# Kernel tuning notes

Hardware: AMD Instinct MI355X
Metric: run time of the kernel (lower is better)

Reference implementation:

```python
import jax, jax.numpy as jnp
import numpy as np


def _hippo_scale_params(N, L):
    """Replicates HiPPOScale.__init__ for discretization='bilinear' (pure numpy)."""
    q = np.arange(N, dtype=np.float64)
    col, row = np.meshgrid(q, q)
    r = 2 * q + 1
    M = -(np.where(row >= col, r, 0) - np.diag(q))
    T = np.sqrt(np.diag(2 * q + 1))
    A = T @ M @ np.linalg.inv(T)          # (N, N)
    B = np.diag(T)                         # (N,)
    ts = np.arange(1, L + 1, dtype=np.float64)[:, None, None]  # (L,1,1)
    At = A[None] / ts                      # A / t, batched over t
    I = np.eye(N, dtype=np.float64)
    Mm = I[None] - 0.5 * At
    Nn = I[None] + 0.5 * At
    A_stacked = np.linalg.solve(Mm, Nn)                      # (L, N, N)
    Bt = B[None, :] / ts[:, 0, :]                             # (L, N)
    B_stacked = np.linalg.solve(Mm, Bt[..., None])[..., 0]    # (L, N)
    return A_stacked.astype(np.float32), B_stacked.astype(np.float32)


def setup_inputs() -> dict:
    N, L, Bsz = 64, 4096, 64
    key = jax.random.key(0)
    A_st, B_st = _hippo_scale_params(N, L)
    inputs = jax.random.normal(key, (L, Bsz), dtype=jnp.float32)
    return {
        "inputs": inputs,                       # (L, B)
        "A_stacked": jnp.asarray(A_st),         # (L, N, N)
        "B_stacked": jnp.asarray(B_st),         # (L, N)
    }


def reference(inputs, A_stacked, B_stacked):
    # u[t, b, :] = inputs[t, b] * B_stacked[t, :]   -> (L, B, N)
    u = inputs[..., None] * B_stacked[:, None, :]

    # x[t] = A[t] @ x[t-1] + u[t], x[-1] = 0  (time-varying linear recurrence).
    # The torch code computes this via a divide-and-conquer unroll; here we use
    # the equivalent parallel associative scan with elements (A, u) and
    # composition (A2@A1, A2@u1 + u2).
    def combine(e1, e2):
        a1, u1 = e1
        a2, u2 = e2
        a = jnp.matmul(a2, a1)                                  # (l, N, N)
        v = jnp.einsum('...ij,...bj->...bi', a2, u1) + u2       # (l, B, N)
        return (a, v)

    _, x = jax.lax.associative_scan(combine, (A_stacked, u))
    return x  # (L, B, N)
```

## Files before the change

### kernel.cpp

```cpp
#include <hip/hip_runtime.h>
#include <hip/hip_bf16.h>

#define TL 4096
#define NB 64
#define CH 8
#define CN 512
#define AS 72

typedef __attribute__((ext_vector_type(8))) short short8;
typedef __attribute__((ext_vector_type(4))) short short4v;
typedef __attribute__((ext_vector_type(4))) float floatx4;
typedef __attribute__((ext_vector_type(4))) unsigned int uint4v;

__device__ inline floatx4 mfma_bf16(short8 a, short8 b, floatx4 c) {
    return __builtin_amdgcn_mfma_f32_16x16x32_bf16(a, b, c, 0, 0, 0);
}

__device__ inline short bf16_rne(float x) {
    union { __hip_bfloat16 b; unsigned short s; } u;
    u.b = __float2bfloat16(x);
    return (short)u.s;
}

__device__ inline void split_bf16(float x, short& h, short& l) {
    h = bf16_rne(x);
    union { unsigned u; float f; } hv; hv.u = ((unsigned)(unsigned short)h) << 16;
    l = bf16_rne(x - hv.f);
}

__global__ __launch_bounds__(256, 2)
void hippo_phase1(const float* __restrict__ inp, const float* __restrict__ Ag,
                  const float* __restrict__ Bst,
                  unsigned* __restrict__ P32, float* __restrict__ VT)
{
    __shared__ short Ah[NB][AS], Al[NB][AS];
    __shared__ short SBh[NB][AS], SBl[NB][AS];
    __shared__ short VBh[NB][AS], VBl[NB][AS];
    __shared__ float btl[NB], itl[NB];

    const int tid  = threadIdx.x;
    const int c    = blockIdx.x;
    const int t0   = c * CH;
    const int w    = tid >> 6, lane = tid & 63;
    const int quad = lane >> 4, l15 = lane & 15;

#pragma unroll
    for (int q = 0; q < 16; ++q) {
        int f = tid + q * 256;
        int n = f >> 6, k = f & 63;
        SBh[n][k] = (n == k) ? (short)0x3F80 : (short)0;
        SBl[n][k] = 0; VBh[n][k] = 0; VBl[n][k] = 0;
    }

    float4 pre[4];
    {
        const float4* Ap = (const float4*)(Ag + (size_t)t0 * 4096);
#pragma unroll
        for (int q = 0; q < 4; ++q) pre[q] = Ap[tid + q * 256];
    }

    floatx4 accS[4], accV[4];

    for (int s = 0; s < CH; ++s) {
        int t = t0 + s;
#pragma unroll
        for (int q = 0; q < 4; ++q) {
            int f = tid + q * 256;
            int m = f >> 4, k0 = (f & 15) * 4;
            float vv[4] = {pre[q].x, pre[q].y, pre[q].z, pre[q].w};
            short4v h4, l4;
#pragma unroll
            for (int r = 0; r < 4; ++r) { short hh, ll; split_bf16(vv[r], hh, ll); h4[r]=hh; l4[r]=ll; }
            *(short4v*)&Ah[m][k0] = h4;
            *(short4v*)&Al[m][k0] = l4;
        }
        if (tid < 64) { btl[tid] = Bst[(size_t)t*64 + tid]; itl[tid] = inp[(size_t)t*64 + tid]; }
        if (s + 1 < CH) {
            const float4* Ap = (const float4*)(Ag + (size_t)(t+1) * 4096);
#pragma unroll
            for (int q = 0; q < 4; ++q) pre[q] = Ap[tid + q * 256];
        }
        __syncthreads();

#pragma unroll
        for (int ni = 0; ni < 4; ++ni) {
            float ib = itl[16*ni + l15];
#pragma unroll
            for (int r = 0; r < 4; ++r) {
                accS[ni][r] = 0.0f;
                accV[ni][r] = btl[16*w + 4*quad + r] * ib;
            }
        }
#pragma unroll
        for (int kc = 0; kc < 2; ++kc) {
            int ko = 32*kc + 8*quad;
            short8 aH = *(const short8*)&Ah[16*w + l15][ko];
            short8 aL = *(const short8*)&Al[16*w + l15][ko];
#pragma unroll
            for (int ni = 0; ni < 4; ++ni) {
                int n = 16*ni + l15;
                short8 sH = *(const short8*)&SBh[n][ko];
                short8 sL = *(const short8*)&SBl[n][ko];
                accS[ni] = mfma_bf16(aH, sH, accS[ni]);
                accS[ni] = mfma_bf16(aH, sL, accS[ni]);
                accS[ni] = mfma_bf16(aL, sH, accS[ni]);
                short8 vH = *(const short8*)&VBh[n][ko];
                short8 vL = *(const short8*)&VBl[n][ko];
                accV[ni] = mfma_bf16(aH, vH, accV[ni]);
                accV[ni] = mfma_bf16(aH, vL, accV[ni]);
                accV[ni] = mfma_bf16(aL, vH, accV[ni]);
            }
        }
        __syncthreads();

        if (s + 1 < CH) {
#pragma unroll
            for (int ni = 0; ni < 4; ++ni) {
                int cc = 16*ni + l15, r0 = 16*w + 4*quad;
                short4v h4, l4;
#pragma unroll
                for (int r = 0; r < 4; ++r) { short hh,ll; split_bf16(accS[ni][r],hh,ll); h4[r]=hh; l4[r]=ll; }
                *(short4v*)&SBh[cc][r0] = h4; *(short4v*)&SBl[cc][r0] = l4;
#pragma unroll
                for (int r = 0; r < 4; ++r) { short hh,ll; split_bf16(accV[ni][r],hh,ll); h4[r]=hh; l4[r]=ll; }
                *(short4v*)&VBh[cc][r0] = h4; *(short4v*)&VBl[cc][r0] = l4;
            }
        }
    }
    unsigned* po = P32 + (size_t)c * 4096;
#pragma unroll
    for (int ni = 0; ni < 4; ++ni) {
        int cc = 16*ni + l15, r0 = 16*w + 4*quad;
        *(floatx4*)(VT + (size_t)c*4096 + cc*64 + r0) = accV[ni];
#pragma unroll
        for (int r = 0; r < 4; ++r) {
            short hh, ll; split_bf16(accS[ni][r], hh, ll);
            po[(r0 + r)*64 + cc] = ((unsigned)(unsigned short)hh << 16) | (unsigned)(unsigned short)ll;
        }
    }
}

__global__ __launch_bounds__(256, 2)
void hippo_seqscan(unsigned* __restrict__ P32, float* __restrict__ VT,
                   int bstride, int off0, int estride)
{
    __shared__ short PAh[NB][AS], PAl[NB][AS];
    __shared__ short PBh[NB][AS], PBl[NB][AS];
    __shared__ short VBh[NB][AS], VBl[NB][AS];

    const int tid  = threadIdx.x;
    const int base = blockIdx.x * bstride + off0;
    const int w    = tid >> 6, lane = tid & 63;
    const int quad = lane >> 4, l15 = lane & 15;

    {
        const unsigned* p0 = P32 + (size_t)base * 4096;
        const float*    v0 = VT  + (size_t)base * 4096;
#pragma unroll
        for (int q = 0; q < 4; ++q) {
            int f = tid + q * 256;
            int k = f & 63, m0 = (f >> 6) * 4;
            uint4v pk = *(const uint4v*)(p0 + k * 64 + m0);
#pragma unroll
            for (int r = 0; r < 4; ++r) {
                PBh[m0 + r][k] = (short)(pk[r] >> 16);
                PBl[m0 + r][k] = (short)(pk[r] & 0xFFFFu);
            }
        }
#pragma unroll
        for (int q = 0; q < 4; ++q) {
            int f = tid + q * 256;
            int n = f >> 4, k0 = (f & 15) * 4;
            float4 vv = *(const float4*)(v0 + n * 64 + k0);
            float va[4] = {vv.x, vv.y, vv.z, vv.w};
            short4v vh4, vl4;
#pragma unroll
            for (int r = 0; r < 4; ++r) { short hh, ll; split_bf16(va[r], hh, ll); vh4[r]=hh; vl4[r]=ll; }
            *(short4v*)&VBh[n][k0] = vh4; *(short4v*)&VBl[n][k0] = vl4;
        }
    }

    uint4v preA[4]; float4 preV[4];
    {
        const unsigned* pc = P32 + (size_t)(base + estride) * 4096;
        const float*    vc = VT  + (size_t)(base + estride) * 4096;
#pragma unroll
        for (int q = 0; q < 4; ++q) {
            int f = tid + q * 256;
            int m = f >> 4, k0 = (f & 15) * 4;
            preA[q] = *(const uint4v*)(pc + m * 64 + k0);
        }
#pragma unroll
        for (int ni = 0; ni < 4; ++ni) {
            int cc = 16 * ni + l15, r0 = 16 * w + 4 * quad;
            preV[ni] = *(const float4*)(vc + cc * 64 + r0);
        }
    }

    for (int i = 1; i < 8; ++i) {
#pragma unroll
        for (int q = 0; q < 4; ++q) {
            int f = tid + q * 256;
            int m = f >> 4, k0 = (f & 15) * 4;
            short4v h4, l4;
#pragma unroll
            for (int r = 0; r < 4; ++r) { h4[r] = (short)(preA[q][r] >> 16); l4[r] = (short)(preA[q][r] & 0xFFFFu); }
            *(short4v*)&PAh[m][k0] = h4;
            *(short4v*)&PAl[m][k0] = l4;
        }
        floatx4 accP[4], accV[4];
#pragma unroll
        for (int ni = 0; ni < 4; ++ni) {
            accV[ni][0] = preV[ni].x; accV[ni][1] = preV[ni].y;
            accV[ni][2] = preV[ni].z; accV[ni][3] = preV[ni].w;
            accP[ni][0] = accP[ni][1] = accP[ni][2] = accP[ni][3] = 0.0f;
        }
        if (i + 1 < 8) {
            const unsigned* pc = P32 + (size_t)(base + (i + 1) * estride) * 4096;
            const float*    vc = VT  + (size_t)(base + (i + 1) * estride) * 4096;
#pragma unroll
            for (int q = 0; q < 4; ++q) {
                int f = tid + q * 256;
                int m = f >> 4, k0 = (f & 15) * 4;
                preA[q] = *(const uint4v*)(pc + m * 64 + k0);
            }
#pragma unroll
            for (int ni = 0; ni < 4; ++ni) {
                int cc = 16 * ni + l15, r0 = 16 * w + 4 * quad;
                preV[ni] = *(const float4*)(vc + cc * 64 + r0);
            }
        }
        __syncthreads();

#pragma unroll
        for (int kc = 0; kc < 2; ++kc) {
            int ko = 32 * kc + 8 * quad;
            short8 aH = *(const short8*)&PAh[16 * w + l15][ko];
            short8 aL = *(const short8*)&PAl[16 * w + l15][ko];
#pragma unroll
            for (int ni = 0; ni < 4; ++ni) {
                int n = 16 * ni + l15;
                short8 pH = *(const short8*)&PBh[n][ko];
                short8 pL = *(const short8*)&PBl[n][ko];
                accP[ni] = mfma_bf16(aH, pH, accP[ni]);
                accP[ni] = mfma_bf16(aH, pL, accP[ni]);
                accP[ni] = mfma_bf16(aL, pH, accP[ni]);
                short8 vH = *(const short8*)&VBh[n][ko];
                short8 vL = *(const short8*)&VBl[n][ko];
                accV[ni] = mfma_bf16(aH, vH, accV[ni]);
                accV[ni] = mfma_bf16(aH, vL, accV[ni]);
                accV[ni] = mfma_bf16(aL, vH, accV[ni]);
            }
        }
        __syncthreads();

        int idx = base + i * estride;
        unsigned* po = P32 + (size_t)idx * 4096;
#pragma unroll
        for (int ni = 0; ni < 4; ++ni) {
            int cc = 16 * ni + l15, r0 = 16 * w + 4 * quad;
            *(floatx4*)(VT + (size_t)idx * 4096 + cc * 64 + r0) = accV[ni];
            short4v h4, l4;
#pragma unroll
            for (int r = 0; r < 4; ++r) {
                short hh, ll; split_bf16(accP[ni][r], hh, ll);
                po[(r0 + r) * 64 + cc] = ((unsigned)(unsigned short)hh << 16) | (unsigned)(unsigned short)ll;
                h4[r] = hh; l4[r] = ll;
            }
            *(short4v*)&PBh[cc][r0] = h4; *(short4v*)&PBl[cc][r0] = l4;
#pragma unroll
            for (int r = 0; r < 4; ++r) { short hh,ll; split_bf16(accV[ni][r],hh,ll); h4[r]=hh; l4[r]=ll; }
            *(short4v*)&VBh[cc][r0] = h4; *(short4v*)&VBl[cc][r0] = l4;
        }
    }
}

__global__ __launch_bounds__(256, 2)
void hippo_s3(unsigned* __restrict__ P32, const float* __restrict__ VT)
{
    __shared__ short PAh[NB][AS], PAl[NB][AS];
    __shared__ short EBh[NB][AS], EBl[NB][AS];
    const int tid = threadIdx.x;
    const int w = tid >> 6, lane = tid & 63, quad = lane >> 4, l15 = lane & 15;

#pragma unroll
    for (int q = 0; q < 16; ++q) {
        int f = tid + q * 256; EBh[f >> 6][f & 63] = 0; EBl[f >> 6][f & 63] = 0;
    }
    for (int s = 0; s < 7; ++s) {
        int idx = 64 * s + 63;
        const unsigned* pc = P32 + (size_t)idx * 4096;
        const float*    vc = VT  + (size_t)idx * 4096;
#pragma unroll
        for (int q = 0; q < 4; ++q) {
            int f = tid + q * 256;
            int m = f >> 4, k0 = (f & 15) * 4;
            uint4v pk = *(const uint4v*)(pc + m * 64 + k0);
            short4v h4, l4;
#pragma unroll
            for (int r = 0; r < 4; ++r) { h4[r] = (short)(pk[r] >> 16); l4[r] = (short)(pk[r] & 0xFFFFu); }
            *(short4v*)&PAh[m][k0] = h4;
            *(short4v*)&PAl[m][k0] = l4;
        }
        floatx4 acc[4];
#pragma unroll
        for (int ni = 0; ni < 4; ++ni) {
            int cc = 16 * ni + l15, r0 = 16 * w + 4 * quad;
            float4 vv = *(const float4*)(vc + cc * 64 + r0);
            acc[ni][0] = vv.x; acc[ni][1] = vv.y; acc[ni][2] = vv.z; acc[ni][3] = vv.w;
        }
        __syncthreads();
#pragma unroll
        for (int kc = 0; kc < 2; ++kc) {
            int ko = 32 * kc + 8 * quad;
            short8 aH = *(const short8*)&PAh[16 * w + l15][ko];
            short8 aL = *(const short8*)&PAl[16 * w + l15][ko];
#pragma unroll
            for (int ni = 0; ni < 4; ++ni) {
                int n = 16 * ni + l15;
                short8 eH = *(const short8*)&EBh[n][ko];
                short8 eL = *(const short8*)&EBl[n][ko];
                acc[ni] = mfma_bf16(aH, eH, acc[ni]);
                acc[ni] = mfma_bf16(aH, eL, acc[ni]);
                acc[ni] = mfma_bf16(aL, eH, acc[ni]);
            }
        }
        __syncthreads();
        float* eo = (float*)(P32 + (size_t)idx * 4096);
#pragma unroll
        for (int ni = 0; ni < 4; ++ni) {
            int cc = 16 * ni + l15, r0 = 16 * w + 4 * quad;
            *(floatx4*)(eo + cc * 64 + r0) = acc[ni];
            short4v h4, l4;
#pragma unroll
            for (int r = 0; r < 4; ++r) { short hh,ll; split_bf16(acc[ni][r],hh,ll); h4[r]=hh; l4[r]=ll; }
            *(short4v*)&EBh[cc][r0] = h4; *(short4v*)&EBl[cc][r0] = l4;
        }
    }
}

__global__ __launch_bounds__(256, 2)
void hippo_phase3(const float* __restrict__ inp, const float* __restrict__ Ag,
                  const float* __restrict__ Bst, const unsigned* __restrict__ P32,
                  const float* __restrict__ VT, float* __restrict__ out)
{
    __shared__ short Ah[NB][AS], Al[NB][AS];
    __shared__ short XBh[NB][AS], XBl[NB][AS];
    __shared__ float btl[NB], itl[NB];

    const int tid = threadIdx.x, c = blockIdx.x, t0 = c * CH;
    const int w = tid>>6, lane = tid&63, quad = lane>>4, l15 = lane&15;
    const int sup = c >> 6, g = c >> 3, gi = g & 7, j = c & 7;

    float4 pre[4];
    {
        const float4* Ap = (const float4*)(Ag + (size_t)t0 * 4096);
#pragma unroll
        for (int q = 0; q < 4; ++q) pre[q] = Ap[tid + q * 256];
    }

    if (sup == 0) {
#pragma unroll
        for (int q = 0; q < 16; ++q) { int f = tid + q*256; XBh[f>>6][f&63] = 0; XBl[f>>6][f&63] = 0; }
    } else {
        const float* e = (const float*)(P32 + (size_t)(64*(sup-1) + 63) * 4096);
#pragma unroll
        for (int q = 0; q < 4; ++q) {
            int f = tid + q*256; int b = f>>4, k0 = (f&15)*4;
            float4 v = *(const float4*)(e + b*64 + k0);
            float va[4] = {v.x,v.y,v.z,v.w};
            short4v h4, l4;
#pragma unroll
            for (int r=0;r<4;++r){short hh,ll;split_bf16(va[r],hh,ll);h4[r]=hh;l4[r]=ll;}
            *(short4v*)&XBh[b][k0] = h4; *(short4v*)&XBl[b][k0] = l4;
        }
    }

    auto combine = [&](int idx) {
        const unsigned* pc = P32 + (size_t)idx * 4096;
        const float*    vc = VT  + (size_t)idx * 4096;
#pragma unroll
        for (int q = 0; q < 4; ++q) {
            int f = tid + q*256;
            int m = f >> 4, k0 = (f & 15) * 4;
            uint4v pk = *(const uint4v*)(pc + m * 64 + k0);
            short4v h4, l4;
#pragma unroll
            for (int r = 0; r < 4; ++r) { h4[r] = (short)(pk[r] >> 16); l4[r] = (short)(pk[r] & 0xFFFFu); }
            *(short4v*)&Ah[m][k0] = h4;
            *(short4v*)&Al[m][k0] = l4;
        }
        floatx4 acc[4];
#pragma unroll
        for (int ni = 0; ni < 4; ++ni) {
            int cc = 16*ni + l15, r0 = 16*w + 4*quad;
            float4 vv = *(const float4*)(vc + cc*64 + r0);
            acc[ni][0]=vv.x; acc[ni][1]=vv.y; acc[ni][2]=vv.z; acc[ni][3]=vv.w;
        }
        __syncthreads();
#pragma unroll
        for (int kc = 0; kc < 2; ++kc) {
            int ko = 32*kc + 8*quad;
            short8 aH = *(const short8*)&Ah[16*w + l15][ko];
            short8 aL = *(const short8*)&Al[16*w + l15][ko];
#pragma unroll
            for (int ni = 0; ni < 4; ++ni) {
                int n = 16*ni + l15;
                short8 xH = *(const short8*)&XBh[n][ko];
                short8 xL = *(const short8*)&XBl[n][ko];
                acc[ni] = mfma_bf16(aH, xH, acc[ni]);
                acc[ni] = mfma_bf16(aH, xL, acc[ni]);
                acc[ni] = mfma_bf16(aL, xH, acc[ni]);
            }
        }
        __syncthreads();
#pragma unroll
        for (int ni = 0; ni < 4; ++ni) {
            int cc = 16*ni + l15, r0 = 16*w + 4*quad;
            short4v h4, l4;
#pragma unroll
            for (int r=0;r<4;++r){short hh,ll;split_bf16(acc[ni][r],hh,ll);h4[r]=hh;l4[r]=ll;}
            *(short4v*)&XBh[cc][r0] = h4; *(short4v*)&XBl[cc][r0] = l4;
        }
    };
    if (gi) combine(8*g - 1);
    if (j)  combine(c - 1);

    floatx4 acc[4];
    for (int s = 0; s < CH; ++s) {
        int t = t0 + s;
#pragma unroll
        for (int q = 0; q < 4; ++q) {
            int f = tid + q*256; int m = f>>4, k0 = (f&15)*4;
            float vv[4] = {pre[q].x,pre[q].y,pre[q].z,pre[q].w};
            short4v h4, l4;
#pragma unroll
            for (int r=0;r<4;++r){short hh,ll;split_bf16(vv[r],hh,ll);h4[r]=hh;l4[r]=ll;}
            *(short4v*)&Ah[m][k0] = h4; *(short4v*)&Al[m][k0] = l4;
        }
        if (tid < 64) { btl[tid] = Bst[(size_t)t*64 + tid]; itl[tid] = inp[(size_t)t*64 + tid]; }
        if (s + 1 < CH) {
            const float4* Ap = (const float4*)(Ag + (size_t)(t+1) * 4096);
#pragma unroll
            for (int q = 0; q < 4; ++q) pre[q] = Ap[tid + q * 256];
        }
        __syncthreads();

#pragma unroll
        for (int ni = 0; ni < 4; ++ni) {
            float ib = itl[16*ni + l15];
#pragma unroll
            for (int r = 0; r < 4; ++r) acc[ni][r] = btl[16*w + 4*quad + r] * ib;
        }
#pragma unroll
        for (int kc = 0; kc < 2; ++kc) {
            int ko = 32*kc + 8*quad;
            short8 aH = *(const short8*)&Ah[16*w + l15][ko];
            short8 aL = *(const short8*)&Al[16*w + l15][ko];
#pragma unroll
            for (int ni = 0; ni < 4; ++ni) {
                int n = 16*ni + l15;
                short8 xH = *(const short8*)&XBh[n][ko];
                short8 xL = *(const short8*)&XBl[n][ko];
                acc[ni] = mfma_bf16(aH, xH, acc[ni]);
                acc[ni] = mfma_bf16(aH, xL, acc[ni]);
                acc[ni] = mfma_bf16(aL, xH, acc[ni]);
            }
        }
        __syncthreads();
#pragma unroll
        for (int ni = 0; ni < 4; ++ni) {
            int cc = 16*ni + l15, r0 = 16*w + 4*quad;
            *(floatx4*)(out + (size_t)t*4096 + cc*64 + r0) = acc[ni];
            if (s + 1 < CH) {
                short4v h4, l4;
#pragma unroll
                for (int r=0;r<4;++r){short hh,ll;split_bf16(acc[ni][r],hh,ll);h4[r]=hh;l4[r]=ll;}
                *(short4v*)&XBh[cc][r0] = h4; *(short4v*)&XBl[cc][r0] = l4;
            }
        }
    }
}

extern "C" void kernel_launch(void* const* d_in, const int* in_sizes, int n_in,
                              void* d_out, int out_size, void* d_ws, size_t ws_size,
                              hipStream_t stream)
{
    const float* inp = (const float*)d_in[0];
    const float* A   = (const float*)d_in[1];
    const float* Bst = (const float*)d_in[2];
    float* out = (float*)d_out;
    float* ws  = (float*)d_ws;

    unsigned* P32 = (unsigned*)ws;
    float*    VT  = ws + (size_t)CN * 4096;

    hippo_phase1<<<CN, 256, 0, stream>>>(inp, A, Bst, P32, VT);
    hippo_seqscan<<<64, 256, 0, stream>>>(P32, VT, 8, 0, 1);
    hippo_seqscan<<<8, 256, 0, stream>>>(P32, VT, 64, 7, 8);
    hippo_s3<<<1, 256, 0, stream>>>(P32, VT);
    hippo_phase3<<<CN, 256, 0, stream>>>(inp, A, Bst, P32, VT, out);
}
```

Before: 184.0 us.

## Load A fragments directly into registers and double-buffer LDS state to halve barriers

Each wave now loads its own A-matrix MFMA fragments straight from global memory into registers and converts them to hi/lo bf16 there, instead of staging A through shared memory. The recurrence state buffers are double-buffered in LDS, so each step needs one __syncthreads instead of two. Phase 1 also skips the first identity multiply by initializing the state directly from A[t0] and B*u. The B and input scalars are now prefetched into registers rather than staged in shared memory. This cuts LDS traffic and barrier stalls, at the cost of twice the state LDS footprint and more registers.

```diff
diff --git a/kernel.cpp b/kernel.cpp
--- a/kernel.cpp
+++ b/kernel.cpp
@@ -15,17 +15,27 @@
 __device__ inline floatx4 mfma_bf16(short8 a, short8 b, floatx4 c) {
     return __builtin_amdgcn_mfma_f32_16x16x32_bf16(a, b, c, 0, 0, 0);
 }
-
 __device__ inline short bf16_rne(float x) {
     union { __hip_bfloat16 b; unsigned short s; } u;
     u.b = __float2bfloat16(x);
     return (short)u.s;
 }
-
 __device__ inline void split_bf16(float x, short& h, short& l) {
     h = bf16_rne(x);
     union { unsigned u; float f; } hv; hv.u = ((unsigned)(unsigned short)h) << 16;
     l = bf16_rne(x - hv.f);
+}
+__device__ inline void cvt_frag(float4 a, float4 b, short8& H, short8& L) {
+    float v[8] = {a.x,a.y,a.z,a.w,b.x,b.y,b.z,b.w};
+#pragma unroll
+    for (int r = 0; r < 8; ++r) { short hh,ll; split_bf16(v[r],hh,ll); H[r]=hh; L[r]=ll; }
+}
+__device__ inline void unpack_frag(uint4v a, uint4v b, short8& H, short8& L) {
+#pragma unroll
+    for (int r = 0; r < 4; ++r) {
+        H[r]   = (short)(a[r] >> 16); L[r]   = (short)(a[r] & 0xFFFFu);
+        H[4+r] = (short)(b[r] >> 16); L[4+r] = (short)(b[r] & 0xFFFFu);
+    }
 }
 
 __global__ __launch_bounds__(256, 2)
@@ -33,109 +43,139 @@
                   const float* __restrict__ Bst,
                   unsigned* __restrict__ P32, float* __restrict__ VT)
 {
-    __shared__ short Ah[NB][AS], Al[NB][AS];
-    __shared__ short SBh[NB][AS], SBl[NB][AS];
-    __shared__ short VBh[NB][AS], VBl[NB][AS];
-    __shared__ float btl[NB], itl[NB];
-
-    const int tid  = threadIdx.x;
-    const int c    = blockIdx.x;
-    const int t0   = c * CH;
-    const int w    = tid >> 6, lane = tid & 63;
+    __shared__ short SBh[2][NB][AS], SBl[2][NB][AS];
+    __shared__ short VBh[2][NB][AS], VBl[2][NB][AS];
+
+    const int tid = threadIdx.x;
+    const int c = blockIdx.x, t0 = c * CH;
+    const int w = tid >> 6, lane = tid & 63;
     const int quad = lane >> 4, l15 = lane & 15;
-
-#pragma unroll
-    for (int q = 0; q < 16; ++q) {
-        int f = tid + q * 256;
-        int n = f >> 6, k = f & 63;
-        SBh[n][k] = (n == k) ? (short)0x3F80 : (short)0;
-        SBl[n][k] = 0; VBh[n][k] = 0; VBl[n][k] = 0;
-    }
-
-    float4 pre[4];
+    const int arow = 16*w + l15;
+    const int wr0  = 16*w + 4*quad;
+
+    float4 rA[2][2];
+#pragma unroll
+    for (int kc = 0; kc < 2; ++kc) {
+        const float* p = Ag + (size_t)(t0+1)*4096 + (size_t)arow*64 + 32*kc + 8*quad;
+        rA[kc][0] = *(const float4*)p;
+        rA[kc][1] = *(const float4*)(p + 4);
+    }
+    float4 bnxt = *(const float4*)(Bst + (size_t)(t0+1)*64 + wr0);
+    float inxt[4];
+#pragma unroll
+    for (int ni = 0; ni < 4; ++ni) inxt[ni] = inp[(size_t)(t0+1)*64 + l15 + 16*ni];
+
+    floatx4 accS[4], accV[4];
     {
-        const float4* Ap = (const float4*)(Ag + (size_t)t0 * 4096);
-#pragma unroll
-        for (int q = 0; q < 4; ++q) pre[q] = Ap[tid + q * 256];
-    }
-
-    floatx4 accS[4], accV[4];
-
-    for (int s = 0; s < CH; ++s) {
-        int t = t0 + s;
-#pragma unroll
-        for (int q = 0; q < 4; ++q) {
-            int f = tid + q * 256;
-            int m = f >> 4, k0 = (f & 15) * 4;
-            float vv[4] = {pre[q].x, pre[q].y, pre[q].z, pre[q].w};
-            short4v h4, l4;
-#pragma unroll
-            for (int r = 0; r < 4; ++r) { short hh, ll; split_bf16(vv[r], hh, ll); h4[r]=hh; l4[r]=ll; }
-            *(short4v*)&Ah[m][k0] = h4;
-            *(short4v*)&Al[m][k0] = l4;
-        }
-        if (tid < 64) { btl[tid] = Bst[(size_t)t*64 + tid]; itl[tid] = inp[(size_t)t*64 + tid]; }
+        const float* A0 = Ag + (size_t)t0 * 4096;
+        float4 b0 = *(const float4*)(Bst + (size_t)t0*64 + wr0);
+        float bc[4] = {b0.x,b0.y,b0.z,b0.w};
+#pragma unroll
+        for (int ni = 0; ni < 4; ++ni) {
+            const float ii = inp[(size_t)t0*64 + l15 + 16*ni];
+#pragma unroll
+            for (int r = 0; r < 4; ++r) {
+                accS[ni][r] = A0[(size_t)(wr0 + r)*64 + l15 + 16*ni];
+                accV[ni][r] = bc[r] * ii;
+            }
+        }
+    }
+#pragma unroll
+    for (int ni = 0; ni < 4; ++ni) {
+        const int cc = l15 + 16*ni;
+        short4v h4, l4;
+#pragma unroll
+        for (int r = 0; r < 4; ++r) { short hh,ll; split_bf16(accS[ni][r],hh,ll); h4[r]=hh; l4[r]=ll; }
+        *(short4v*)&SBh[0][cc][wr0] = h4; *(short4v*)&SBl[0][cc][wr0] = l4;
+#pragma unroll
+        for (int r = 0; r < 4; ++r) { short hh,ll; split_bf16(accV[ni][r],hh,ll); h4[r]=hh; l4[r]=ll; }
+        *(short4v*)&VBh[0][cc][wr0] = h4; *(short4v*)&VBl[0][cc][wr0] = l4;
+    }
+    __syncthreads();
+
+    short8 aH[2], aL[2];
+#pragma unroll
+    for (int kc = 0; kc < 2; ++kc) cvt_frag(rA[kc][0], rA[kc][1], aH[kc], aL[kc]);
+
+    int cur = 0;
+    float4 bcur = bnxt;
+    float icur[4];
+#pragma unroll
+    for (int ni = 0; ni < 4; ++ni) icur[ni] = inxt[ni];
+
+    for (int s = 1; s < CH; ++s) {
         if (s + 1 < CH) {
-            const float4* Ap = (const float4*)(Ag + (size_t)(t+1) * 4096);
-#pragma unroll
-            for (int q = 0; q < 4; ++q) pre[q] = Ap[tid + q * 256];
-        }
-        __syncthreads();
-
-#pragma unroll
-        for (int ni = 0; ni < 4; ++ni) {
-            float ib = itl[16*ni + l15];
+            const int t1 = t0 + s + 1;
+#pragma unroll
+            for (int kc = 0; kc < 2; ++kc) {
+                const float* p = Ag + (size_t)t1*4096 + (size_t)arow*64 + 32*kc + 8*quad;
+                rA[kc][0] = *(const float4*)p;
+                rA[kc][1] = *(const float4*)(p + 4);
+            }
+            bnxt = *(const float4*)(Bst + (size_t)t1*64 + wr0);
+#pragma unroll
+            for (int ni = 0; ni < 4; ++ni) inxt[ni] = inp[(size_t)t1*64 + l15 + 16*ni];
+        }
+        {
+            float bc[4] = {bcur.x,bcur.y,bcur.z,bcur.w};
+#pragma unroll
+            for (int ni = 0; ni < 4; ++ni)
 #pragma unroll
             for (int r = 0; r < 4; ++r) {
                 accS[ni][r] = 0.0f;
-                accV[ni][r] = btl[16*w + 4*quad + r] * ib;
-            }
-        }
-#pragma unroll
-        for (int kc = 0; kc < 2; ++kc) {
-            int ko = 32*kc + 8*quad;
-            short8 aH = *(const short8*)&Ah[16*w + l15][ko];
-            short8 aL = *(const short8*)&Al[16*w + l15][ko];
+                accV[ni][r] = bc[r] * icur[ni];
+            }
+        }
+#pragma unroll
+        for (int kc = 0; kc < 2; ++kc) {
+            const int ko = 32*kc + 8*quad;
 #pragma unroll
             for (int ni = 0; ni < 4; ++ni) {
-                int n = 16*ni + l15;
-                short8 sH = *(const short8*)&SBh[n][ko];
-                short8 sL = *(const short8*)&SBl[n][ko];
-                accS[ni] = mfma_bf16(aH, sH, accS[ni]);
-                accS[ni] = mfma_bf16(aH, sL, accS[ni]);
-                accS[ni] = mfma_bf16(aL, sH, accS[ni]);
-                short8 vH = *(const short8*)&VBh[n][ko];
-                short8 vL = *(const short8*)&VBl[n][ko];
-                accV[ni] = mfma_bf16(aH, vH, accV[ni]);
-                accV[ni] = mfma_bf16(aH, vL, accV[ni]);
-                accV[ni] = mfma_bf16(aL, vH, accV[ni]);
-            }
-        }
-        __syncthreads();
-
+                const int n = l15 + 16*ni;
+                short8 sH = *(const short8*)&SBh[cur][n][ko];
+                short8 sL = *(const short8*)&SBl[cur][n][ko];
+                short8 vH = *(const short8*)&VBh[cur][n][ko];
+                short8 vL = *(const short8*)&VBl[cur][n][ko];
+                accS[ni] = mfma_bf16(aH[kc], sH, accS[ni]);
+                accS[ni] = mfma_bf16(aH[kc], sL, accS[ni]);
+                accS[ni] = mfma_bf16(aL[kc], sH, accS[ni]);
+                accV[ni] = mfma_bf16(aH[kc], vH, accV[ni]);
+                accV[ni] = mfma_bf16(aH[kc], vL, accV[ni]);
+                accV[ni] = mfma_bf16(aL[kc], vH, accV[ni]);
+            }
+        }
         if (s + 1 < CH) {
 #pragma unroll
+            for (int kc = 0; kc < 2; ++kc) cvt_frag(rA[kc][0], rA[kc][1], aH[kc], aL[kc]);
+            const int nb = cur ^ 1;
+#pragma unroll
             for (int ni = 0; ni < 4; ++ni) {
-                int cc = 16*ni + l15, r0 = 16*w + 4*quad;
+                const int cc = l15 + 16*ni;
                 short4v h4, l4;
 #pragma unroll
                 for (int r = 0; r < 4; ++r) { short hh,ll; split_bf16(accS[ni][r],hh,ll); h4[r]=hh; l4[r]=ll; }
-                *(short4v*)&SBh[cc][r0] = h4; *(short4v*)&SBl[cc][r0] = l4;
+                *(short4v*)&SBh[nb][cc][wr0] = h4; *(short4v*)&SBl[nb][cc][wr0] = l4;
 #pragma unroll
                 for (int r = 0; r < 4; ++r) { short hh,ll; split_bf16(accV[ni][r],hh,ll); h4[r]=hh; l4[r]=ll; }
-                *(short4v*)&VBh[cc][r0] = h4; *(short4v*)&VBl[cc][r0] = l4;
-            }
-        }
-    }
+                *(short4v*)&VBh[nb][cc][wr0] = h4; *(short4v*)&VBl[nb][cc][wr0] = l4;
+            }
+            __syncthreads();
+            cur ^= 1;
+        }
+        bcur = bnxt;
+#pragma unroll
+        for (int ni = 0; ni < 4; ++ni) icur[ni] = inxt[ni];
+    }
+
     unsigned* po = P32 + (size_t)c * 4096;
 #pragma unroll
     for (int ni = 0; ni < 4; ++ni) {
-        int cc = 16*ni + l15, r0 = 16*w + 4*quad;
-        *(floatx4*)(VT + (size_t)c*4096 + cc*64 + r0) = accV[ni];
+        const int cc = l15 + 16*ni;
+        *(floatx4*)(VT + (size_t)c*4096 + cc*64 + wr0) = accV[ni];
 #pragma unroll
         for (int r = 0; r < 4; ++r) {
             short hh, ll; split_bf16(accS[ni][r], hh, ll);
-            po[(r0 + r)*64 + cc] = ((unsigned)(unsigned short)hh << 16) | (unsigned)(unsigned short)ll;
+            po[(size_t)(wr0 + r)*64 + cc] = ((unsigned)(unsigned short)hh << 16) | (unsigned)(unsigned short)ll;
         }
     }
 }
@@ -144,14 +184,15 @@
 void hippo_seqscan(unsigned* __restrict__ P32, float* __restrict__ VT,
                    int bstride, int off0, int estride)
 {
-    __shared__ short PAh[NB][AS], PAl[NB][AS];
-    __shared__ short PBh[NB][AS], PBl[NB][AS];
-    __shared__ short VBh[NB][AS], VBl[NB][AS];
-
-    const int tid  = threadIdx.x;
+    __shared__ short PBh[2][NB][AS], PBl[2][NB][AS];
+    __shared__ short VBh[2][NB][AS], VBl[2][NB][AS];
+
+    const int tid = threadIdx.x;
     const int base = blockIdx.x * bstride + off0;
-    const int w    = tid >> 6, lane = tid & 63;
+    const int w = tid >> 6, lane = tid & 63;
     const int quad = lane >> 4, l15 = lane & 15;
+    const int arow = 16*w + l15;
+    const int wr0  = 16*w + 4*quad;
 
     {
         const unsigned* p0 = P32 + (size_t)base * 4096;
@@ -163,8 +204,8 @@
             uint4v pk = *(const uint4v*)(p0 + k * 64 + m0);
 #pragma unroll
             for (int r = 0; r < 4; ++r) {
-                PBh[m0 + r][k] = (short)(pk[r] >> 16);
-                PBl[m0 + r][k] = (short)(pk[r] & 0xFFFFu);
+                PBh[0][m0 + r][k] = (short)(pk[r] >> 16);
+                PBl[0][m0 + r][k] = (short)(pk[r] & 0xFFFFu);
             }
         }
 #pragma unroll
@@ -176,166 +217,188 @@
             short4v vh4, vl4;
 #pragma unroll
             for (int r = 0; r < 4; ++r) { short hh, ll; split_bf16(va[r], hh, ll); vh4[r]=hh; vl4[r]=ll; }
-            *(short4v*)&VBh[n][k0] = vh4; *(short4v*)&VBl[n][k0] = vl4;
-        }
-    }
-
-    uint4v preA[4]; float4 preV[4];
+            *(short4v*)&VBh[0][n][k0] = vh4; *(short4v*)&VBl[0][n][k0] = vl4;
+        }
+    }
+    uint4v rP[2][2]; float4 preV[4];
     {
         const unsigned* pc = P32 + (size_t)(base + estride) * 4096;
         const float*    vc = VT  + (size_t)(base + estride) * 4096;
 #pragma unroll
-        for (int q = 0; q < 4; ++q) {
-            int f = tid + q * 256;
-            int m = f >> 4, k0 = (f & 15) * 4;
-            preA[q] = *(const uint4v*)(pc + m * 64 + k0);
-        }
-#pragma unroll
-        for (int ni = 0; ni < 4; ++ni) {
-            int cc = 16 * ni + l15, r0 = 16 * w + 4 * quad;
-            preV[ni] = *(const float4*)(vc + cc * 64 + r0);
-        }
-    }
-
+        for (int kc = 0; kc < 2; ++kc) {
+            const unsigned* p = pc + (size_t)arow*64 + 32*kc + 8*quad;
+            rP[kc][0] = *(const uint4v*)p;
+            rP[kc][1] = *(const uint4v*)(p + 4);
+        }
+#pragma unroll
+        for (int ni = 0; ni < 4; ++ni)
+            preV[ni] = *(const float4*)(vc + (size_t)(l15 + 16*ni)*64 + wr0);
+    }
+    __syncthreads();
+
+    short8 aH[2], aL[2];
+#pragma unroll
+    for (int kc = 0; kc < 2; ++kc) unpack_frag(rP[kc][0], rP[kc][1], aH[kc], aL[kc]);
+
+    int cur = 0;
     for (int i = 1; i < 8; ++i) {
-#pragma unroll
-        for (int q = 0; q < 4; ++q) {
-            int f = tid + q * 256;
-            int m = f >> 4, k0 = (f & 15) * 4;
-            short4v h4, l4;
-#pragma unroll
-            for (int r = 0; r < 4; ++r) { h4[r] = (short)(preA[q][r] >> 16); l4[r] = (short)(preA[q][r] & 0xFFFFu); }
-            *(short4v*)&PAh[m][k0] = h4;
-            *(short4v*)&PAl[m][k0] = l4;
-        }
+        const int idx = base + i * estride;
         floatx4 accP[4], accV[4];
 #pragma unroll
         for (int ni = 0; ni < 4; ++ni) {
             accV[ni][0] = preV[ni].x; accV[ni][1] = preV[ni].y;
             accV[ni][2] = preV[ni].z; accV[ni][3] = preV[ni].w;
-            accP[ni][0] = accP[ni][1] = accP[ni][2] = accP[ni][3] = 0.0f;
+            accP[ni][0]=accP[ni][1]=accP[ni][2]=accP[ni][3]=0.0f;
         }
         if (i + 1 < 8) {
-            const unsigned* pc = P32 + (size_t)(base + (i + 1) * estride) * 4096;
-            const float*    vc = VT  + (size_t)(base + (i + 1) * estride) * 4096;
-#pragma unroll
-            for (int q = 0; q < 4; ++q) {
-                int f = tid + q * 256;
-                int m = f >> 4, k0 = (f & 15) * 4;
-                preA[q] = *(const uint4v*)(pc + m * 64 + k0);
-            }
+            const unsigned* pc = P32 + (size_t)(base + (i+1) * estride) * 4096;
+            const float*    vc = VT  + (size_t)(base + (i+1) * estride) * 4096;
+#pragma unroll
+            for (int kc = 0; kc < 2; ++kc) {
+                const unsigned* p = pc + (size_t)arow*64 + 32*kc + 8*quad;
+                rP[kc][0] = *(const uint4v*)p;
+                rP[kc][1] = *(const uint4v*)(p + 4);
+            }
+#pragma unroll
+            for (int ni = 0; ni < 4; ++ni)
+                preV[ni] = *(const float4*)(vc + (size_t)(l15 + 16*ni)*64 + wr0);
+        }
+#pragma unroll
+        for (int kc = 0; kc < 2; ++kc) {
+            const int ko = 32*kc + 8*quad;
 #pragma unroll
             for (int ni = 0; ni < 4; ++ni) {
-                int cc = 16 * ni + l15, r0 = 16 * w + 4 * quad;
-                preV[ni] = *(const float4*)(vc + cc * 64 + r0);
-            }
-        }
-        __syncthreads();
-
-#pragma unroll
-        for (int kc = 0; kc < 2; ++kc) {
-            int ko = 32 * kc + 8 * quad;
-            short8 aH = *(const short8*)&PAh[16 * w + l15][ko];
-            short8 aL = *(const short8*)&PAl[16 * w + l15][ko];
-#pragma unroll
-            for (int ni = 0; ni < 4; ++ni) {
-                int n = 16 * ni + l15;
-                short8 pH = *(const short8*)&PBh[n][ko];
-                short8 pL = *(const short8*)&PBl[n][ko];
-                accP[ni] = mfma_bf16(aH, pH, accP[ni]);
-                accP[ni] = mfma_bf16(aH, pL, accP[ni]);
-                accP[ni] = mfma_bf16(aL, pH, accP[ni]);
-                short8 vH = *(const short8*)&VBh[n][ko];
-                short8 vL = *(const short8*)&VBl[n][ko];
-                accV[ni] = mfma_bf16(aH, vH, accV[ni]);
-                accV[ni] = mfma_bf16(aH, vL, accV[ni]);
-                accV[ni] = mfma_bf16(aL, vH, accV[ni]);
-            }
-        }
-        __syncthreads();
-
-        int idx = base + i * estride;
+                const int n = l15 + 16*ni;
+                short8 pH = *(const short8*)&PBh[cur][n][ko];
+                short8 pL = *(const short8*)&PBl[cur][n][ko];
+                short8 vH = *(const short8*)&VBh[cur][n][ko];
+                short8 vL = *(const short8*)&VBl[cur][n][ko];
+                accP[ni] = mfma_bf16(aH[kc], pH, accP[ni]);
+                accP[ni] = mfma_bf16(aH[kc], pL, accP[ni]);
+                accP[ni] = mfma_bf16(aL[kc], pH, accP[ni]);
+                accV[ni] = mfma_bf16(aH[kc], vH, accV[ni]);
+                accV[ni] = mfma_bf16(aH[kc], vL, accV[ni]);
+                accV[ni] = mfma_bf16(aL[kc], vH, accV[ni]);
+            }
+        }
+        if (i + 1 < 8) {
+#pragma unroll
+            for (int kc = 0; kc < 2; ++kc) unpack_frag(rP[kc][0], rP[kc][1], aH[kc], aL[kc]);
+        }
         unsigned* po = P32 + (size_t)idx * 4096;
-#pragma unroll
-        for (int ni = 0; ni < 4; ++ni) {
-            int cc = 16 * ni + l15, r0 = 16 * w + 4 * quad;
-            *(floatx4*)(VT + (size_t)idx * 4096 + cc * 64 + r0) = accV[ni];
+        const int nb = cur ^ 1;
+#pragma unroll
+        for (int ni = 0; ni < 4; ++ni) {
+            const int cc = l15 + 16*ni;
+            *(floatx4*)(VT + (size_t)idx*4096 + cc*64 + wr0) = accV[ni];
             short4v h4, l4;
 #pragma unroll
             for (int r = 0; r < 4; ++r) {
                 short hh, ll; split_bf16(accP[ni][r], hh, ll);
-                po[(r0 + r) * 64 + cc] = ((unsigned)(unsigned short)hh << 16) | (unsigned)(unsigned short)ll;
-                h4[r] = hh; l4[r] = ll;
-            }
-            *(short4v*)&PBh[cc][r0] = h4; *(short4v*)&PBl[cc][r0] = l4;
-#pragma unroll
-            for (int r = 0; r < 4; ++r) { short hh,ll; split_bf16(accV[ni][r],hh,ll); h4[r]=hh; l4[r]=ll; }
-            *(short4v*)&VBh[cc][r0] = h4; *(short4v*)&VBl[cc][r0] = l4;
-        }
+                po[(size_t)(wr0+r)*64 + cc] = ((unsigned)(unsigned short)hh << 16) | (unsigned)(unsigned short)ll;
+                h4[r]=hh; l4[r]=ll;
+            }
+            if (i + 1 < 8) {
+                *(short4v*)&PBh[nb][cc][wr0] = h4; *(short4v*)&PBl[nb][cc][wr0] = l4;
+                short4v vh4, vl4;
+#pragma unroll
+                for (int r = 0; r < 4; ++r) { short hh,ll; split_bf16(accV[ni][r],hh,ll); vh4[r]=hh; vl4[r]=ll; }
+                *(short4v*)&VBh[nb][cc][wr0] = vh4; *(short4v*)&VBl[nb][cc][wr0] = vl4;
+            }
+        }
+        if (i + 1 < 8) __syncthreads();
+        cur ^= 1;
     }
 }
 
 __global__ __launch_bounds__(256, 2)
 void hippo_s3(unsigned* __restrict__ P32, const float* __restrict__ VT)
 {
-    __shared__ short PAh[NB][AS], PAl[NB][AS];
-    __shared__ short EBh[NB][AS], EBl[NB][AS];
+    __shared__ short EBh[2][NB][AS], EBl[2][NB][AS];
     const int tid = threadIdx.x;
     const int w = tid >> 6, lane = tid & 63, quad = lane >> 4, l15 = lane & 15;
+    const int arow = 16*w + l15;
+    const int wr0  = 16*w + 4*quad;
 
 #pragma unroll
     for (int q = 0; q < 16; ++q) {
-        int f = tid + q * 256; EBh[f >> 6][f & 63] = 0; EBl[f >> 6][f & 63] = 0;
-    }
+        int f = tid + q * 256; EBh[0][f >> 6][f & 63] = 0; EBl[0][f >> 6][f & 63] = 0;
+    }
+    uint4v rP[2][2]; float4 preV[4];
+    {
+        const unsigned* pc = P32 + (size_t)63 * 4096;
+        const float*    vc = VT  + (size_t)63 * 4096;
+#pragma unroll
+        for (int kc = 0; kc < 2; ++kc) {
+            const unsigned* p = pc + (size_t)arow*64 + 32*kc + 8*quad;
+            rP[kc][0] = *(const uint4v*)p;
+            rP[kc][1] = *(const uint4v*)(p + 4);
+        }
+#pragma unroll
+        for (int ni = 0; ni < 4; ++ni)
+            preV[ni] = *(const float4*)(vc + (size_t)(l15 + 16*ni)*64 + wr0);
+    }
+    __syncthreads();
+
+    short8 aH[2], aL[2];
+#pragma unroll
+    for (int kc = 0; kc < 2; ++kc) unpack_frag(rP[kc][0], rP[kc][1], aH[kc], aL[kc]);
+
+    int cur = 0;
     for (int s = 0; s < 7; ++s) {
-        int idx = 64 * s + 63;
-        const unsigned* pc = P32 + (size_t)idx * 4096;
-        const float*    vc = VT  + (size_t)idx * 4096;
-#pragma unroll
-        for (int q = 0; q < 4; ++q) {
-            int f = tid + q * 256;
-            int m = f >> 4, k0 = (f & 15) * 4;
-            uint4v pk = *(const uint4v*)(pc + m * 64 + k0);
-            short4v h4, l4;
-#pragma unroll
-            for (int r = 0; r < 4; ++r) { h4[r] = (short)(pk[r] >> 16); l4[r] = (short)(pk[r] & 0xFFFFu); }
-            *(short4v*)&PAh[m][k0] = h4;
-            *(short4v*)&PAl[m][k0] = l4;
-        }
+        const int idx = 64 * s + 63;
         floatx4 acc[4];
 #pragma unroll
         for (int ni = 0; ni < 4; ++ni) {
-            int cc = 16 * ni + l15, r0 = 16 * w + 4 * quad;
-            float4 vv = *(const float4*)(vc + cc * 64 + r0);
-            acc[ni][0] = vv.x; acc[ni][1] = vv.y; acc[ni][2] = vv.z; acc[ni][3] = vv.w;
-        }
-        __syncthreads();
-#pragma unroll
-        for (int kc = 0; kc < 2; ++kc) {
-            int ko = 32 * kc + 8 * quad;
-            short8 aH = *(const short8*)&PAh[16 * w + l15][ko];
-            short8 aL = *(const short8*)&PAl[16 * w + l15][ko];
+            acc[ni][0] = preV[ni].x; acc[ni][1] = preV[ni].y;
+            acc[ni][2] = preV[ni].z; acc[ni][3] = preV[ni].w;
+        }
+        if (s + 1 < 7) {
+            const int idx2 = 64 * (s + 1) + 63;
+            const unsigned* pc = P32 + (size_t)idx2 * 4096;
+            const float*    vc = VT  + (size_t)idx2 * 4096;
+#pragma unroll
+            for (int kc = 0; kc < 2; ++kc) {
+                const unsigned* p = pc + (size_t)arow*64 + 32*kc + 8*quad;
+                rP[kc][0] = *(const uint4v*)p;
+                rP[kc][1] = *(const uint4v*)(p + 4);
+            }
+#pragma unroll
+            for (int ni = 0; ni < 4; ++ni)
+                preV[ni] = *(const float4*)(vc + (size_t)(l15 + 16*ni)*64 + wr0);
+        }
+#pragma unroll
+        for (int kc = 0; kc < 2; ++kc) {
+            const int ko = 32*kc + 8*quad;
 #pragma unroll
             for (int ni = 0; ni < 4; ++ni) {
-                int n = 16 * ni + l15;
-                short8 eH = *(const short8*)&EBh[n][ko];
-                short8 eL = *(const short8*)&EBl[n][ko];
-                acc[ni] = mfma_bf16(aH, eH, acc[ni]);
-                acc[ni] = mfma_bf16(aH, eL, acc[ni]);
-                acc[ni] = mfma_bf16(aL, eH, acc[ni]);
-            }
-        }
-        __syncthreads();
+                const int n = l15 + 16*ni;
+                short8 eH = *(const short8*)&EBh[cur][n][ko];
+                short8 eL = *(const short8*)&EBl[cur][n][ko];
+                acc[ni] = mfma_bf16(aH[kc], eH, acc[ni]);
+                acc[ni] = mfma_bf16(aH[kc], eL, acc[ni]);
+                acc[ni] = mfma_bf16(aL[kc], eH, acc[ni]);
+            }
+        }
+        if (s + 1 < 7) {
+#pragma unroll
+            for (int kc = 0; kc < 2; ++kc) unpack_frag(rP[kc][0], rP[kc][1], aH[kc], aL[kc]);
+        }
         float* eo = (float*)(P32 + (size_t)idx * 4096);
-#pragma unroll
-        for (int ni = 0; ni < 4; ++ni) {
-            int cc = 16 * ni + l15, r0 = 16 * w + 4 * quad;
-            *(floatx4*)(eo + cc * 64 + r0) = acc[ni];
-            short4v h4, l4;
-#pragma unroll
-            for (int r = 0; r < 4; ++r) { short hh,ll; split_bf16(acc[ni][r],hh,ll); h4[r]=hh; l4[r]=ll; }
-            *(short4v*)&EBh[cc][r0] = h4; *(short4v*)&EBl[cc][r0] = l4;
-        }
+        const int nb = cur ^ 1;
+#pragma unroll
+        for (int ni = 0; ni < 4; ++ni) {
+            const int cc = l15 + 16*ni;
+            *(floatx4*)(eo + cc*64 + wr0) = acc[ni];
+            if (s + 1 < 7) {
+                short4v h4, l4;
+#pragma unroll
+                for (int r = 0; r < 4; ++r) { short hh,ll; split_bf16(acc[ni][r],hh,ll); h4[r]=hh; l4[r]=ll; }
+                *(short4v*)&EBh[nb][cc][wr0] = h4; *(short4v*)&EBl[nb][cc][wr0] = l4;
+            }
+        }
+        if (s + 1 < 7) __syncthreads();
+        cur ^= 1;
     }
 }
 
@@ -344,24 +407,29 @@
                   const float* __restrict__ Bst, const unsigned* __restrict__ P32,
                   const float* __restrict__ VT, float* __restrict__ out)
 {
-    __shared__ short Ah[NB][AS], Al[NB][AS];
-    __shared__ short XBh[NB][AS], XBl[NB][AS];
-    __shared__ float btl[NB], itl[NB];
+    __shared__ short XBh[2][NB][AS], XBl[2][NB][AS];
 
     const int tid = threadIdx.x, c = blockIdx.x, t0 = c * CH;
-    const int w = tid>>6, lane = tid&63, quad = lane>>4, l15 = lane&15;
+    const int w = tid >> 6, lane = tid & 63, quad = lane >> 4, l15 = lane & 15;
+    const int arow = 16*w + l15;
+    const int wr0  = 16*w + 4*quad;
     const int sup = c >> 6, g = c >> 3, gi = g & 7, j = c & 7;
 
-    float4 pre[4];
-    {
-        const float4* Ap = (const float4*)(Ag + (size_t)t0 * 4096);
-#pragma unroll
-        for (int q = 0; q < 4; ++q) pre[q] = Ap[tid + q * 256];
-    }
+    float4 rA[2][2];
+#pragma unroll
+    for (int kc = 0; kc < 2; ++kc) {
+        const float* p = Ag + (size_t)t0*4096 + (size_t)arow*64 + 32*kc + 8*quad;
+        rA[kc][0] = *(const float4*)p;
+        rA[kc][1] = *(const float4*)(p + 4);
+    }
+    float4 bcur = *(const float4*)(Bst + (size_t)t0*64 + wr0);
+    float icur[4];
+#pragma unroll
+    for (int ni = 0; ni < 4; ++ni) icur[ni] = inp[(size_t)t0*64 + l15 + 16*ni];
 
     if (sup == 0) {
 #pragma unroll
-        for (int q = 0; q < 16; ++q) { int f = tid + q*256; XBh[f>>6][f&63] = 0; XBl[f>>6][f&63] = 0; }
+        for (int q = 0; q < 16; ++q) { int f = tid + q*256; XBh[0][f>>6][f&63] = 0; XBl[0][f>>6][f&63] = 0; }
     } else {
         const float* e = (const float*)(P32 + (size_t)(64*(sup-1) + 63) * 4096);
 #pragma unroll
@@ -372,113 +440,119 @@
             short4v h4, l4;
 #pragma unroll
             for (int r=0;r<4;++r){short hh,ll;split_bf16(va[r],hh,ll);h4[r]=hh;l4[r]=ll;}
-            *(short4v*)&XBh[b][k0] = h4; *(short4v*)&XBl[b][k0] = l4;
-        }
-    }
+            *(short4v*)&XBh[0][b][k0] = h4; *(short4v*)&XBl[0][b][k0] = l4;
+        }
+    }
+    __syncthreads();
+    int cur = 0;
 
     auto combine = [&](int idx) {
+        uint4v rP[2][2];
         const unsigned* pc = P32 + (size_t)idx * 4096;
         const float*    vc = VT  + (size_t)idx * 4096;
 #pragma unroll
-        for (int q = 0; q < 4; ++q) {
-            int f = tid + q*256;
-            int m = f >> 4, k0 = (f & 15) * 4;
-            uint4v pk = *(const uint4v*)(pc + m * 64 + k0);
+        for (int kc = 0; kc < 2; ++kc) {
+            const unsigned* p = pc + (size_t)arow*64 + 32*kc + 8*quad;
+            rP[kc][0] = *(const uint4v*)p;
+            rP[kc][1] = *(const uint4v*)(p + 4);
+        }
+        floatx4 acc[4];
+#pragma unroll
+        for (int ni = 0; ni < 4; ++ni) {
+            float4 vv = *(const float4*)(vc + (size_t)(l15 + 16*ni)*64 + wr0);
+            acc[ni][0]=vv.x; acc[ni][1]=vv.y; acc[ni][2]=vv.z; acc[ni][3]=vv.w;
+        }
+        short8 cH[2], cL[2];
+#pragma unroll
+        for (int kc = 0; kc < 2; ++kc) unpack_frag(rP[kc][0], rP[kc][1], cH[kc], cL[kc]);
+#pragma unroll
+        for (int kc = 0; kc < 2; ++kc) {
+            const int ko = 32*kc + 8*quad;
+#pragma unroll
+            for (int ni = 0; ni < 4; ++ni) {
+                const int n = l15 + 16*ni;
+                short8 xH = *(const short8*)&XBh[cur][n][ko];
+                short8 xL = *(const short8*)&XBl[cur][n][ko];
+                acc[ni] = mfma_bf16(cH[kc], xH, acc[ni]);
+                acc[ni] = mfma_bf16(cH[kc], xL, acc[ni]);
+                acc[ni] = mfma_bf16(cL[kc], xH, acc[ni]);
+            }
+        }
+        const int nb = cur ^ 1;
+#pragma unroll
+        for (int ni = 0; ni < 4; ++ni) {
+            const int cc = l15 + 16*ni;
             short4v h4, l4;
 #pragma unroll
-            for (int r = 0; r < 4; ++r) { h4[r] = (short)(pk[r] >> 16); l4[r] = (short)(pk[r] & 0xFFFFu); }
-            *(short4v*)&Ah[m][k0] = h4;
-            *(short4v*)&Al[m][k0] = l4;
-        }
-        floatx4 acc[4];
-#pragma unroll
-        for (int ni = 0; ni < 4; ++ni) {
-            int cc = 16*ni + l15, r0 = 16*w + 4*quad;
-            float4 vv = *(const float4*)(vc + cc*64 + r0);
-            acc[ni][0]=vv.x; acc[ni][1]=vv.y; acc[ni][2]=vv.z; acc[ni][3]=vv.w;
+            for (int r=0;r<4;++r){short hh,ll;split_bf16(acc[ni][r],hh,ll);h4[r]=hh;l4[r]=ll;}
+            *(short4v*)&XBh[nb][cc][wr0] = h4; *(short4v*)&XBl[nb][cc][wr0] = l4;
         }
         __syncthreads();
-#pragma unroll
-        for (int kc = 0; kc < 2; ++kc) {
-            int ko = 32*kc + 8*quad;
-            short8 aH = *(const short8*)&Ah[16*w + l15][ko];
-            short8 aL = *(const short8*)&Al[16*w + l15][ko];
-#pragma unroll
-            for (int ni = 0; ni < 4; ++ni) {
-                int n = 16*ni + l15;
-                short8 xH = *(const short8*)&XBh[n][ko];
-                short8 xL = *(const short8*)&XBl[n][ko];
-                acc[ni] = mfma_bf16(aH, xH, acc[ni]);
-                acc[ni] = mfma_bf16(aH, xL, acc[ni]);
-                acc[ni] = mfma_bf16(aL, xH, acc[ni]);
-            }
-        }
-        __syncthreads();
-#pragma unroll
-        for (int ni = 0; ni < 4; ++ni) {
-            int cc = 16*ni + l15, r0 = 16*w + 4*quad;
-            short4v h4, l4;
-#pragma unroll
-            for (int r=0;r<4;++r){short hh,ll;split_bf16(acc[ni][r],hh,ll);h4[r]=hh;l4[r]=ll;}
-            *(short4v*)&XBh[cc][r0] = h4; *(short4v*)&XBl[cc][r0] = l4;
-        }
+        cur ^= 1;
     };
     if (gi) combine(8*g - 1);
     if (j)  combine(c - 1);
 
+    short8 aH[2], aL[2];
+#pragma unroll
+    for (int kc = 0; kc < 2; ++kc) cvt_frag(rA[kc][0], rA[kc][1], aH[kc], aL[kc]);
+
+    float4 bnxt; float inxt[4];
     floatx4 acc[4];
     for (int s = 0; s < CH; ++s) {
-        int t = t0 + s;
-#pragma unroll
-        for (int q = 0; q < 4; ++q) {
-            int f = tid + q*256; int m = f>>4, k0 = (f&15)*4;
-            float vv[4] = {pre[q].x,pre[q].y,pre[q].z,pre[q].w};
-            short4v h4, l4;
-#pragma unroll
-            for (int r=0;r<4;++r){short hh,ll;split_bf16(vv[r],hh,ll);h4[r]=hh;l4[r]=ll;}
-            *(short4v*)&Ah[m][k0] = h4; *(short4v*)&Al[m][k0] = l4;
-        }
-        if (tid < 64) { btl[tid] = Bst[(size_t)t*64 + tid]; itl[tid] = inp[(size_t)t*64 + tid]; }
+        const int t = t0 + s;
         if (s + 1 < CH) {
-            const float4* Ap = (const float4*)(Ag + (size_t)(t+1) * 4096);
-#pragma unroll
-            for (int q = 0; q < 4; ++q) pre[q] = Ap[tid + q * 256];
-        }
-        __syncthreads();
-
-#pragma unroll
-        for (int ni = 0; ni < 4; ++ni) {
-            float ib = itl[16*ni + l15];
-#pragma unroll
-            for (int r = 0; r < 4; ++r) acc[ni][r] = btl[16*w + 4*quad + r] * ib;
-        }
-#pragma unroll
-        for (int kc = 0; kc < 2; ++kc) {
-            int ko = 32*kc + 8*quad;
-            short8 aH = *(const short8*)&Ah[16*w + l15][ko];
-            short8 aL = *(const short8*)&Al[16*w + l15][ko];
+            const int t1 = t + 1;
+#pragma unroll
+            for (int kc = 0; kc < 2; ++kc) {
+                const float* p = Ag + (size_t)t1*4096 + (size_t)arow*64 + 32*kc + 8*quad;
+                rA[kc][0] = *(const float4*)p;
+                rA[kc][1] = *(const float4*)(p + 4);
+            }
+            bnxt = *(const float4*)(Bst + (size_t)t1*64 + wr0);
+#pragma unroll
+            for (int ni = 0; ni < 4; ++ni) inxt[ni] = inp[(size_t)t1*64 + l15 + 16*ni];
+        }
+        {
+            float bc[4] = {bcur.x,bcur.y,bcur.z,bcur.w};
+#pragma unroll
+            for (int ni=0;ni<4;++ni)
+#pragma unroll
+            for (int r=0;r<4;++r) acc[ni][r] = bc[r] * icur[ni];
+        }
+#pragma unroll
+        for (int kc = 0; kc < 2; ++kc) {
+            const int ko = 32*kc + 8*quad;
 #pragma unroll
             for (int ni = 0; ni < 4; ++ni) {
-                int n = 16*ni + l15;
-                short8 xH = *(const short8*)&XBh[n][ko];
-                short8 xL = *(const short8*)&XBl[n][ko];
-                acc[ni] = mfma_bf16(aH, xH, acc[ni]);
-                acc[ni] = mfma_bf16(aH, xL, acc[ni]);
-                acc[ni] = mfma_bf16(aL, xH, acc[ni]);
-            }
-        }
-        __syncthreads();
-#pragma unroll
-        for (int ni = 0; ni < 4; ++ni) {
-            int cc = 16*ni + l15, r0 = 16*w + 4*quad;
-            *(floatx4*)(out + (size_t)t*4096 + cc*64 + r0) = acc[ni];
+                const int n = l15 + 16*ni;
+                short8 xH = *(const short8*)&XBh[cur][n][ko];
+                short8 xL = *(const short8*)&XBl[cur][n][ko];
+                acc[ni] = mfma_bf16(aH[kc], xH, acc[ni]);
+                acc[ni] = mfma_bf16(aH[kc], xL, acc[ni]);
+                acc[ni] = mfma_bf16(aL[kc], xH, acc[ni]);
+            }
+        }
+        if (s + 1 < CH) {
+#pragma unroll
+            for (int kc = 0; kc < 2; ++kc) cvt_frag(rA[kc][0], rA[kc][1], aH[kc], aL[kc]);
+        }
+        const int nb = cur ^ 1;
+#pragma unroll
+        for (int ni = 0; ni < 4; ++ni) {
+            const int cc = l15 + 16*ni;
+            *(floatx4*)(out + (size_t)t*4096 + cc*64 + wr0) = acc[ni];
             if (s + 1 < CH) {
                 short4v h4, l4;
 #pragma unroll
                 for (int r=0;r<4;++r){short hh,ll;split_bf16(acc[ni][r],hh,ll);h4[r]=hh;l4[r]=ll;}
-                *(short4v*)&XBh[cc][r0] = h4; *(short4v*)&XBl[cc][r0] = l4;
-            }
-        }
+                *(short4v*)&XBh[nb][cc][wr0] = h4; *(short4v*)&XBl[nb][cc][wr0] = l4;
+            }
+        }
+        if (s + 1 < CH) { __syncthreads(); cur ^= 1; }
+        bcur = bnxt;
+#pragma unroll
+        for (int ni = 0; ni < 4; ++ni) icur[ni] = inxt[ni];
     }
 }
 
```

New measurement: 183.9 us. About the same (-0.1%).
